# Kernel tuning notes

Measured on AMD Instinct MI355X. Metric: run time of the kernel, lower is better.

The kernel has to match this reference:

```python
import jax, jax.numpy as jnp
from jax import lax
import numpy as np

B, T = 512, 64
VOCAB, EMB, HID, NIMG = 10000, 512, 1024, 2048


def setup_inputs() -> dict:
    key = jax.random.key(0)
    ks = jax.random.split(key, 8)
    s_ih = 1.0 / np.sqrt(HID)
    return {
        "m": jax.random.randint(ks[0], (B, T), 0, VOCAB),
        "emb": jax.random.normal(ks[1], (VOCAB, EMB), dtype=jnp.float32),
        "W_ih": jax.random.uniform(ks[2], (4 * HID, EMB), minval=-s_ih, maxval=s_ih, dtype=jnp.float32),
        "W_hh": jax.random.uniform(ks[3], (4 * HID, HID), minval=-s_ih, maxval=s_ih, dtype=jnp.float32),
        "b_ih": jax.random.uniform(ks[4], (4 * HID,), minval=-s_ih, maxval=s_ih, dtype=jnp.float32),
        "b_hh": jax.random.uniform(ks[5], (4 * HID,), minval=-s_ih, maxval=s_ih, dtype=jnp.float32),
        "W_out": jax.random.normal(ks[6], (NIMG, HID), dtype=jnp.float32) * (1.0 / np.sqrt(HID)),
        "b_out": jnp.zeros((NIMG,), dtype=jnp.float32),
    }


def reference(m, emb, W_ih, W_hh, b_ih, b_hh, W_out, b_out):
    # m: [B, T] int tokens. Embed all steps at once, scan over time.
    x = emb[m]                      # [B, T, E]
    x = jnp.swapaxes(x, 0, 1)       # [T, B, E] (matches m.permute(1,0) step order)
    Bsz = m.shape[0]
    H = W_hh.shape[1]
    h0 = jnp.zeros((Bsz, H), dtype=emb.dtype)
    c0 = jnp.zeros((Bsz, H), dtype=emb.dtype)

    def step(carry, xt):
        h, c = carry
        # PyTorch LSTMCell gate order: input, forget, cell(g), output
        gates = xt @ W_ih.T + b_ih + h @ W_hh.T + b_hh  # [B, 4H]
        i, f, g, o = jnp.split(gates, 4, axis=-1)
        i = jax.nn.sigmoid(i)
        f = jax.nn.sigmoid(f)
        g = jnp.tanh(g)
        o = jax.nn.sigmoid(o)
        c = f * c + i * g
        h = o * jnp.tanh(c)
        return (h, c), None

    (h, _), _ = lax.scan(step, (h0, c0), x)
    return h @ W_out.T + b_out      # [B, n_image_features]
```

## Files before the change

kernel.cpp:

```cpp
#include <hip/hip_runtime.h>
#include <cstdint>

#define B_    512
#define T_    64
#define VOCAB_ 10000
#define VPAD_ 10112
#define EMB_  512
#define HID_  1024
#define G4H_  4096
#define KCAT_ 1536
#define NIMG_ 2048

typedef _Float16 half8 __attribute__((ext_vector_type(8)));
typedef _Float16 half4 __attribute__((ext_vector_type(4)));
typedef float floatx4 __attribute__((ext_vector_type(4)));

__device__ __forceinline__ void async_copy16(void* lds_uniform, const void* gsrc) {
    __builtin_amdgcn_global_load_lds(
        (__attribute__((address_space(1))) void*)(uintptr_t)gsrc,
        (__attribute__((address_space(3))) void*)(uint32_t)(uintptr_t)lds_uniform,
        16, 0, 0);
}

__device__ __forceinline__ float fsig(float x)  { return 1.0f / (1.0f + __expf(-x)); }
__device__ __forceinline__ float ftanh(float x) { return 1.0f - 2.0f / (__expf(2.0f * x) + 1.0f); }


__global__ __launch_bounds__(256) void convert_kernel(
    const int* __restrict__ m, const float* __restrict__ emb,
    const float* __restrict__ W_ih, const float* __restrict__ W_hh,
    const float* __restrict__ b_ih, const float* __restrict__ b_hh,
    const float* __restrict__ W_out,
    _Float16* __restrict__ emb16, _Float16* __restrict__ Wc16,
    _Float16* __restrict__ Wout16, float* __restrict__ biasp,
    _Float16* __restrict__ Hseq, int* __restrict__ tokperm)
{
    const long long EMB_N = (long long)VOCAB_ * EMB_;
    const long long WC_N  = (long long)G4H_ * KCAT_;
    const long long WO_N  = (long long)NIMG_ * HID_;
    const long long BI_N  = G4H_;
    const long long ST_N  = (long long)B_ * HID_;
    const long long TK_N  = (long long)B_ * T_;

    long long i = (long long)blockIdx.x * 256 + threadIdx.x;
    if (i < EMB_N) { emb16[i] = (_Float16)emb[i]; return; }
    i -= EMB_N;
    if (i < WC_N) {
        int n_perm = (int)(i / KCAT_);
        int k      = (int)(i % KCAT_);
        int gate = (n_perm >> 4) & 3;
        int j    = (n_perm >> 6) * 16 + (n_perm & 15);
        int n_orig = gate * HID_ + j;
        float v = (k < EMB_) ? W_ih[(size_t)n_orig * EMB_ + k]
                             : W_hh[(size_t)n_orig * HID_ + (k - EMB_)];
        Wc16[i] = (_Float16)v;
        return;
    }
    i -= WC_N;
    if (i < WO_N) { Wout16[i] = (_Float16)W_out[i]; return; }
    i -= WO_N;
    if (i < BI_N) {
        int n_perm = (int)i;
        int gate = (n_perm >> 4) & 3;
        int j    = (n_perm >> 6) * 16 + (n_perm & 15);
        biasp[i] = b_ih[gate * HID_ + j] + b_hh[gate * HID_ + j];
        return;
    }
    i -= BI_N;
    if (i < ST_N) { Hseq[i] = (_Float16)0.0f; return; }
    i -= ST_N;
    if (i < TK_N) {
        int t = (int)(i / B_), b = (int)(i % B_);
        tokperm[i] = m[(size_t)b * T_ + t];
    }
}

__global__ __launch_bounds__(256) void gemm_pe(
    const _Float16* __restrict__ emb16, const _Float16* __restrict__ Wc16,
    const float* __restrict__ biasp, _Float16* __restrict__ PEx)
{
    __shared__ __align__(16) _Float16 As[128 * 32];
    __shared__ __align__(16) _Float16 Bs[128 * 32];

    const int tid  = threadIdx.x;
    const int wid  = tid >> 6;
    const int lane = tid & 63;
    const int lcol = lane & 15;
    const int quad = lane >> 4;
    const int wm   = wid >> 1;
    const int wn   = wid & 1;

    const int r0 = blockIdx.x * 128;
    const int n0 = blockIdx.y * 128;

    floatx4 acc[4][4];
#pragma unroll
    for (int i = 0; i < 4; ++i)
#pragma unroll
        for (int j = 0; j < 4; ++j) acc[i][j] = (floatx4){0.f, 0.f, 0.f, 0.f};

    const int ar = tid >> 2;
    const int kq = tid & 3;

    for (int k0 = 0; k0 < EMB_; k0 += 32) {
        async_copy16((char*)As + (wid << 10),
                     emb16 + (size_t)(r0 + ar) * EMB_ + (k0 + kq * 8));
        async_copy16((char*)As + 4096 + (wid << 10),
                     emb16 + (size_t)(r0 + 64 + ar) * EMB_ + (k0 + kq * 8));
        async_copy16((char*)Bs + (wid << 10),
                     Wc16 + (size_t)(n0 + ar) * KCAT_ + (k0 + kq * 8));
        async_copy16((char*)Bs + 4096 + (wid << 10),
                     Wc16 + (size_t)(n0 + 64 + ar) * KCAT_ + (k0 + kq * 8));
        __syncthreads();

        half8 af[4], bf[4];
#pragma unroll
        for (int mi = 0; mi < 4; ++mi)
            af[mi] = *(const half8*)&As[(wm * 64 + mi * 16 + lcol) * 32 + quad * 8];
#pragma unroll
        for (int ni = 0; ni < 4; ++ni)
            bf[ni] = *(const half8*)&Bs[(wn * 64 + ni * 16 + lcol) * 32 + quad * 8];
#pragma unroll
        for (int mi = 0; mi < 4; ++mi)
#pragma unroll
            for (int ni = 0; ni < 4; ++ni)
                acc[mi][ni] = __builtin_amdgcn_mfma_f32_16x16x32_f16(
                    af[mi], bf[ni], acc[mi][ni], 0, 0, 0);
        __syncthreads();
    }

    const int jblk = (n0 + wn * 64) >> 6;
    float bv[4];
#pragma unroll
    for (int ni = 0; ni < 4; ++ni) bv[ni] = biasp[n0 + wn * 64 + ni * 16 + lcol];
#pragma unroll
    for (int mi = 0; mi < 4; ++mi) {
#pragma unroll
        for (int r = 0; r < 4; ++r) {
            const int row = r0 + wm * 64 + mi * 16 + quad * 4 + r;
            half4 v;
#pragma unroll
            for (int ni = 0; ni < 4; ++ni)
                v[ni] = (_Float16)(acc[mi][ni][r] + bv[ni]);
            *(half4*)(PEx + (size_t)row * G4H_ + jblk * 64 + lcol * 4) = v;
        }
    }
}

__global__ __launch_bounds__(256, 1) void lstm_persistent(
    const _Float16* __restrict__ PEx, const int* __restrict__ tokperm,
    const _Float16* __restrict__ Wc16,
    _Float16* __restrict__ Hseq,
    unsigned* __restrict__ flags)
{
    __shared__ __align__(16) char Wlds[131072];

    const int tid  = threadIdx.x;
    const int wid  = tid >> 6;
    const int lane = tid & 63;
    const int lcol = lane & 15;
    const int quad = lane >> 4;
    const int bx   = blockIdx.x;
    const int b0   = bx * 128;
    const int by   = blockIdx.y;
    const int n0   = by * 64;

    __builtin_amdgcn_fence(__ATOMIC_ACQUIRE, "agent");

    for (int si = 0; si < 8; ++si) {
        const int s = wid * 8 + si;
#pragma unroll
        for (int g = 0; g < 4; ++g) {
            half8 v = *(const half8*)(Wc16 + (size_t)(n0 + g * 16 + lcol) * KCAT_
                                      + EMB_ + s * 32 + quad * 8);
            *(half8*)(Wlds + (((s * 4 + g) << 6) + lane) * 16) = v;
        }
    }

    float cst[2][4] = {{0.f, 0.f, 0.f, 0.f}, {0.f, 0.f, 0.f, 0.f}};
    half4 pe[2][4];

#pragma unroll
    for (int mi = 0; mi < 2; ++mi)
#pragma unroll
        for (int r = 0; r < 4; ++r) {
            const int row = wid * 32 + mi * 16 + quad * 4 + r;
            const int tk = tokperm[b0 + row];
            pe[mi][r] = *(const half4*)(PEx + (size_t)tk * G4H_ + by * 64 + lcol * 4);
        }

    __syncthreads();

    const int wrow = wid * 32;

    for (int t = 0; t < T_; ++t) {
        const _Float16* h_prev = Hseq + (size_t)t * (B_ * HID_);
        _Float16*       h_next = Hseq + (size_t)(t + 1) * (B_ * HID_);

        if (t > 0) {
            const unsigned want = 0x5AB00000u + (unsigned)(t - 1);
            const unsigned* f = flags + ((size_t)(t - 1) * 4 + bx) * 64;
            while (!__all((int)(__hip_atomic_load(&f[lane], __ATOMIC_RELAXED,
                                                  __HIP_MEMORY_SCOPE_AGENT) == want)))
                __builtin_amdgcn_s_sleep(1);
            asm volatile("" ::: "memory");
        }

        const _Float16* arow0 = h_prev + (size_t)(b0 + wrow + lcol) * HID_ + quad * 8;
        const _Float16* arow1 = arow0 + (size_t)16 * HID_;

        floatx4 acc[2][4];
#pragma unroll
        for (int mi = 0; mi < 2; ++mi)
#pragma unroll
            for (int g = 0; g < 4; ++g)
#pragma unroll
                for (int r = 0; r < 4; ++r)
                    acc[mi][g][r] = (float)pe[mi][r][g];

        half8 pa0[8], pa1[8];
#pragma unroll
        for (int i = 0; i < 8; ++i) {
            pa0[i] = *(const half8*)(arow0 + i * 32);
            pa1[i] = *(const half8*)(arow1 + i * 32);
        }
#pragma unroll
        for (int s = 0; s < 32; ++s) {
            const half8 a0 = pa0[s & 7];
            const half8 a1 = pa1[s & 7];
            if (s + 8 < 32) {
                pa0[s & 7] = *(const half8*)(arow0 + (s + 8) * 32);
                pa1[s & 7] = *(const half8*)(arow1 + (s + 8) * 32);
            }
#pragma unroll
            for (int g = 0; g < 4; ++g) {
                const half8 bw = *(const half8*)(Wlds + (((s * 4 + g) << 6) + lane) * 16);
                acc[0][g] = __builtin_amdgcn_mfma_f32_16x16x32_f16(a0, bw, acc[0][g], 0, 0, 0);
                acc[1][g] = __builtin_amdgcn_mfma_f32_16x16x32_f16(a1, bw, acc[1][g], 0, 0, 0);
            }
        }

#pragma unroll
        for (int mi = 0; mi < 2; ++mi)
#pragma unroll
            for (int r = 0; r < 4; ++r) {
                const int row = wrow + mi * 16 + quad * 4 + r;
                const float iv = fsig(acc[mi][0][r]);
                const float fv = fsig(acc[mi][1][r]);
                const float gv = ftanh(acc[mi][2][r]);
                const float ov = fsig(acc[mi][3][r]);
                cst[mi][r] = fv * cst[mi][r] + iv * gv;
                const _Float16 hv = (_Float16)(ov * ftanh(cst[mi][r]));
                unsigned short us = __builtin_bit_cast(unsigned short, hv);
                __hip_atomic_store(
                    (unsigned short*)&h_next[(size_t)(b0 + row) * HID_ + by * 16 + lcol],
                    us, __ATOMIC_RELAXED, __HIP_MEMORY_SCOPE_AGENT);
            }

        __syncthreads();
        if (tid == 0) {
            __hip_atomic_store(&flags[((size_t)t * 4 + bx) * 64 + by],
                               0x5AB00000u + (unsigned)t,
                               __ATOMIC_RELAXED, __HIP_MEMORY_SCOPE_AGENT);
        }

        if (t + 1 < T_) {
#pragma unroll
            for (int mi = 0; mi < 2; ++mi)
#pragma unroll
                for (int r = 0; r < 4; ++r) {
                    const int row = wrow + mi * 16 + quad * 4 + r;
                    const int tk = tokperm[(t + 1) * B_ + b0 + row];
                    pe[mi][r] = *(const half4*)(PEx + (size_t)tk * G4H_ + by * 64 + lcol * 4);
                }
        }
    }
}

__global__ __launch_bounds__(256) void gemm_out(
    const _Float16* __restrict__ A, const _Float16* __restrict__ Bw,
    const float* __restrict__ bias, float* __restrict__ Out, int N, int K)
{
    __shared__ __align__(16) _Float16 As[64 * 32];
    __shared__ __align__(16) _Float16 Bs[128 * 32];

    const int tid  = threadIdx.x;
    const int wid  = tid >> 6;
    const int lane = tid & 63;
    const int lcol = lane & 15;
    const int quad = lane >> 4;
    const int wm   = wid >> 1;
    const int wn   = wid & 1;

    const int b0 = blockIdx.x * 64;
    const int n0 = blockIdx.y * 128;

    floatx4 acc[2][4];
#pragma unroll
    for (int i = 0; i < 2; ++i)
#pragma unroll
        for (int j = 0; j < 4; ++j) acc[i][j] = (floatx4){0.f, 0.f, 0.f, 0.f};

    const int ar = tid >> 2;
    const int kq = tid & 3;

    for (int k0 = 0; k0 < K; k0 += 32) {
        async_copy16((char*)As + (wid << 10), A + (size_t)(b0 + ar) * K + (k0 + kq * 8));
        async_copy16((char*)Bs + (wid << 10), Bw + (size_t)(n0 + ar) * K + (k0 + kq * 8));
        async_copy16((char*)Bs + 4096 + (wid << 10),
                     Bw + (size_t)(n0 + 64 + ar) * K + (k0 + kq * 8));
        __syncthreads();

        half8 af[2], bfr[4];
#pragma unroll
        for (int mi = 0; mi < 2; ++mi)
            af[mi] = *(const half8*)&As[(wm * 32 + mi * 16 + lcol) * 32 + quad * 8];
#pragma unroll
        for (int ni = 0; ni < 4; ++ni)
            bfr[ni] = *(const half8*)&Bs[(wn * 64 + ni * 16 + lcol) * 32 + quad * 8];
#pragma unroll
        for (int mi = 0; mi < 2; ++mi)
#pragma unroll
            for (int ni = 0; ni < 4; ++ni)
                acc[mi][ni] = __builtin_amdgcn_mfma_f32_16x16x32_f16(
                    af[mi], bfr[ni], acc[mi][ni], 0, 0, 0);
        __syncthreads();
    }

#pragma unroll
    for (int mi = 0; mi < 2; ++mi) {
#pragma unroll
        for (int ni = 0; ni < 4; ++ni) {
            const int row = b0 + wm * 32 + mi * 16 + quad * 4;
            const int col = n0 + wn * 64 + ni * 16 + lcol;
            const float bv = bias[col];
#pragma unroll
            for (int r = 0; r < 4; ++r)
                Out[(size_t)(row + r) * N + col] = acc[mi][ni][r] + bv;
        }
    }
}

extern "C" void kernel_launch(void* const* d_in, const int* in_sizes, int n_in,
                              void* d_out, int out_size, void* d_ws, size_t ws_size,
                              hipStream_t stream)
{
    const int*   m     = (const int*)d_in[0];
    const float* emb   = (const float*)d_in[1];
    const float* W_ih  = (const float*)d_in[2];
    const float* W_hh  = (const float*)d_in[3];
    const float* b_ih  = (const float*)d_in[4];
    const float* b_hh  = (const float*)d_in[5];
    const float* W_out = (const float*)d_in[6];
    const float* b_out = (const float*)d_in[7];
    float* out = (float*)d_out;

    char* w = (char*)d_ws;
    size_t off = 0;
    auto alloc = [&](size_t bytes) {
        char* p = w + off;
        off = (off + bytes + 255) & ~(size_t)255;
        return p;
    };
    _Float16* emb16   = (_Float16*)alloc((size_t)VPAD_ * EMB_ * 2);
    _Float16* Wc16    = (_Float16*)alloc((size_t)G4H_ * KCAT_ * 2);
    _Float16* Wout16  = (_Float16*)alloc((size_t)NIMG_ * HID_ * 2);
    float*    biasp   = (float*)   alloc((size_t)G4H_ * 4);
    _Float16* Hseq    = (_Float16*)alloc((size_t)(T_ + 1) * B_ * HID_ * 2);
    int*      tokperm = (int*)     alloc((size_t)B_ * T_ * 4);
    unsigned* flags   = (unsigned*)alloc((size_t)T_ * 4 * 64 * 4);
    _Float16* PEx     = (_Float16*)alloc((size_t)VPAD_ * G4H_ * 2);

    {
        const long long total = (long long)VOCAB_ * EMB_ + (long long)G4H_ * KCAT_ +
                                (long long)NIMG_ * HID_ + G4H_ +
                                (long long)B_ * HID_ + (long long)B_ * T_;
        convert_kernel<<<(int)((total + 255) / 256), 256, 0, stream>>>(
            m, emb, W_ih, W_hh, b_ih, b_hh, W_out,
            emb16, Wc16, Wout16, biasp, Hseq, tokperm);
    }

    gemm_pe<<<dim3(VPAD_ / 128, G4H_ / 128), 256, 0, stream>>>(
        emb16, Wc16, biasp, PEx);

    lstm_persistent<<<dim3(B_ / 128, G4H_ / 64), 256, 0, stream>>>(
        PEx, tokperm, Wc16, Hseq, flags);

    gemm_out<<<dim3(B_ / 64, NIMG_ / 128), 256, 0, stream>>>(
        Hseq + (size_t)T_ * B_ * HID_, Wout16, b_out, out, NIMG_, HID_);
}
```

Measured before the change: 870.7 us.

## Replace whole-step flag barrier with per-chunk readiness waits in LSTM recurrence

Before each time step, the persistent LSTM kernel used to wait until all 64 producer flags for the previous step were set. It now polls the flags with a ballot and waits only for the two flags that cover the K-chunk about to be loaded. Each block starts its K loop at a different offset (by), so blocks whose chunks are already published can begin MFMA work early. The aim is to overlap cross-block synchronisation with compute. The cost is more polling, uniform branches inside the unrolled loop, and a rotated access into the LDS weights.

```diff
diff --git a/kernel.cpp b/kernel.cpp
--- a/kernel.cpp
+++ b/kernel.cpp
@@ -197,14 +197,10 @@
         const _Float16* h_prev = Hseq + (size_t)t * (B_ * HID_);
         _Float16*       h_next = Hseq + (size_t)(t + 1) * (B_ * HID_);
 
-        if (t > 0) {
-            const unsigned want = 0x5AB00000u + (unsigned)(t - 1);
-            const unsigned* f = flags + ((size_t)(t - 1) * 4 + bx) * 64;
-            while (!__all((int)(__hip_atomic_load(&f[lane], __ATOMIC_RELAXED,
-                                                  __HIP_MEMORY_SCOPE_AGENT) == want)))
-                __builtin_amdgcn_s_sleep(1);
-            asm volatile("" ::: "memory");
-        }
+        const unsigned want = 0x5AB00000u + (unsigned)(t - 1);
+        const unsigned* f = flags + ((size_t)(t > 0 ? t - 1 : 0) * 4 + bx) * 64;
+
+        unsigned long long rdy = (t == 0) ? ~0ull : 0ull;
 
         const _Float16* arow0 = h_prev + (size_t)(b0 + wrow + lcol) * HID_ + quad * 8;
         const _Float16* arow1 = arow0 + (size_t)16 * HID_;
@@ -218,23 +214,39 @@
                 for (int r = 0; r < 4; ++r)
                     acc[mi][g][r] = (float)pe[mi][r][g];
 
+        auto waitp = [&](int p) {
+            if (((rdy >> (2 * p)) & 3ull) == 3ull) return;
+            for (;;) {
+                rdy = __ballot((int)(__hip_atomic_load(&f[lane], __ATOMIC_RELAXED,
+                                                       __HIP_MEMORY_SCOPE_AGENT) == want));
+                if (((rdy >> (2 * p)) & 3ull) == 3ull) break;
+                __builtin_amdgcn_s_sleep(1);
+            }
+            asm volatile("" ::: "memory");
+        };
+
         half8 pa0[8], pa1[8];
 #pragma unroll
-        for (int i = 0; i < 8; ++i) {
-            pa0[i] = *(const half8*)(arow0 + i * 32);
-            pa1[i] = *(const half8*)(arow1 + i * 32);
+        for (int c = 0; c < 8; ++c) {
+            const int cs = (c + by) & 31;
+            waitp(cs);
+            pa0[c] = *(const half8*)(arow0 + cs * 32);
+            pa1[c] = *(const half8*)(arow1 + cs * 32);
         }
 #pragma unroll
         for (int s = 0; s < 32; ++s) {
+            const int cs = (s + by) & 31;
             const half8 a0 = pa0[s & 7];
             const half8 a1 = pa1[s & 7];
             if (s + 8 < 32) {
-                pa0[s & 7] = *(const half8*)(arow0 + (s + 8) * 32);
-                pa1[s & 7] = *(const half8*)(arow1 + (s + 8) * 32);
+                const int cs8 = (s + 8 + by) & 31;
+                waitp(cs8);
+                pa0[s & 7] = *(const half8*)(arow0 + cs8 * 32);
+                pa1[s & 7] = *(const half8*)(arow1 + cs8 * 32);
             }
 #pragma unroll
             for (int g = 0; g < 4; ++g) {
-                const half8 bw = *(const half8*)(Wlds + (((s * 4 + g) << 6) + lane) * 16);
+                const half8 bw = *(const half8*)(Wlds + (((cs * 4 + g) << 6) + lane) * 16);
                 acc[0][g] = __builtin_amdgcn_mfma_f32_16x16x32_f16(a0, bw, acc[0][g], 0, 0, 0);
                 acc[1][g] = __builtin_amdgcn_mfma_f32_16x16x32_f16(a1, bw, acc[1][g], 0, 0, 0);
             }
```

After: 953.4 us. +9.5%, slower.
